# Kernel tuning notes

Measured on AMD Instinct MI355X. Metric: run time of the kernel, lower is better.

## Reference

```python
import jax, jax.numpy as jnp
import numpy as np
from jax import lax

T = 8  # hardcoded temporal length in the torch module

def _dwconv_t(z, w, b):
    # z: (N, C, T, 1); w: (C, 1, k, 1) depthwise; 'same' padding along T
    k = w.shape[2]
    p = (k - 1) // 2
    out = lax.conv_general_dilated(
        z, w, window_strides=(1, 1), padding=[(p, p), (0, 0)],
        feature_group_count=z.shape[1],
        dimension_numbers=('NCHW', 'OIHW', 'NCHW'))
    return out + b[None, :, None, None]


def setup_inputs() -> dict:
    key = jax.random.key(0)
    ks = jax.random.split(key, 13)
    C, IC, H, W, B = 1024, 512, 14, 14, 16
    s = lambda k, shp, scale: jax.random.normal(k, shp, dtype=jnp.float32) * scale
    return {
        'x':   s(ks[0], (B * T, C, H, W), 1.0),
        'w1':  s(ks[1], (IC, C, 1, 1), 0.03),
        'b1':  s(ks[2], (IC,), 0.02),
        'wb1': s(ks[3], (IC, 1, 1, 1), 0.3),
        'bb1': s(ks[4], (IC,), 0.02),
        'wb2': s(ks[5], (IC, 1, 3, 1), 0.3),
        'bb2': s(ks[6], (IC,), 0.02),
        'wb3': s(ks[7], (IC, 1, 5, 1), 0.3),
        'bb3': s(ks[8], (IC,), 0.02),
        'wb4': s(ks[9], (IC, 1, 7, 1), 0.3),
        'bb4': s(ks[10], (IC,), 0.02),
        'w2':  s(ks[11], (C, IC, 1, 1), 0.03),
        'b2':  s(ks[12], (C,), 0.02),
    }


def reference(x, w1, b1, wb1, bb1, wb2, bb2, wb3, bb3, wb4, bb4, w2, b2):
    BT, C, H, W = x.shape
    B = BT // T
    IC = w1.shape[0]
    # conv1: 1x1 pointwise conv == channel GEMM
    y = jnp.einsum('nchw,oc->nohw', x, w1[:, :, 0, 0]) + b1[None, :, None, None]
    # (B*T, IC, H, W) -> (B, T, IC, H, W) -> (B, H, W, IC, T) -> (B*H*W, IC, T, 1)
    z = y.reshape(B, T, IC, H, W).transpose(0, 3, 4, 2, 1).reshape(B * H * W, IC, T, 1)
    out = (_dwconv_t(z, wb1, bb1) + _dwconv_t(z, wb2, bb2)
           + _dwconv_t(z, wb3, bb3) + _dwconv_t(z, wb4, bb4))
    # (B*H*W, IC, T, 1) -> (B, H, W, IC, T) -> (B, T, IC, H, W) -> (B*T, IC, H, W)
    out = out.reshape(B, H, W, IC, T).transpose(0, 4, 3, 1, 2).reshape(BT, IC, H, W)
    # conv2: 1x1 pointwise conv back to C channels
    out = jnp.einsum('nihw,oi->nohw', out, w2[:, :, 0, 0]) + b2[None, :, None, None]
    return x + out
```

## Files before the change

kernel.cpp:

```cpp
#include <hip/hip_runtime.h>
#include <hip/hip_bf16.h>

typedef short short8 __attribute__((ext_vector_type(8)));
typedef float f32x4 __attribute__((ext_vector_type(4)));
typedef unsigned int uint;

#define CB   16
#define TT   8
#define CIN  1024
#define ICH  512
#define HWS  196
#define NPB  1568
#define NF   25088

static __device__ __forceinline__ unsigned short f2bf(float f) {
  __hip_bfloat16 h = __float2bfloat16(f); unsigned short u; __builtin_memcpy(&u, &h, 2); return u;
}

static __device__ __forceinline__ void stage16(const void* g, void* l) {
  __builtin_amdgcn_global_load_lds(
      (const __attribute__((address_space(1))) unsigned int*)(unsigned long long)g,
      (__attribute__((address_space(3))) unsigned int*)(unsigned int)(unsigned long long)l,
      16, 0, 0);
}

__global__ void k_prep(const float* __restrict__ x, __hip_bfloat16* __restrict__ xbT,
    const float* __restrict__ w1, const float* __restrict__ w2,
    const float* __restrict__ wb1, const float* __restrict__ bb1,
    const float* __restrict__ wb2, const float* __restrict__ bb2,
    const float* __restrict__ wb3, const float* __restrict__ bb3,
    const float* __restrict__ wb4, const float* __restrict__ bb4,
    __hip_bfloat16* __restrict__ w1b, __hip_bfloat16* __restrict__ w2b,
    float* __restrict__ weff, float* __restrict__ beff) {
  int bid = blockIdx.x;
  if (bid >= CB * TT * 16 * 4) {
    int idx = (bid - CB * TT * 16 * 4) * 256 + threadIdx.x;
    if (idx < CIN * ICH) {
      w1b[idx] = __float2bfloat16(w1[idx]);
      w2b[idx] = __float2bfloat16(w2[idx]);
    }
    if (idx < ICH) {
      float e[7];
#pragma unroll
      for (int u = 0; u < 7; u++) e[u] = wb4[idx * 7 + u];
#pragma unroll
      for (int u = 0; u < 5; u++) e[u + 1] += wb3[idx * 5 + u];
#pragma unroll
      for (int u = 0; u < 3; u++) e[u + 2] += wb2[idx * 3 + u];
      e[3] += wb1[idx];
#pragma unroll
      for (int u = 0; u < 7; u++) weff[idx * 8 + u] = e[u];
      weff[idx * 8 + 7] = 0.f;
      beff[idx] = bb1[idx] + bb2[idx] + bb3[idx] + bb4[idx];
    }
    return;
  }
  __shared__ float tile[64][51];
  int ht = bid & 3;
  int ct = (bid >> 2) & 15;
  int t  = (bid >> 6) & 7;
  int b  = bid >> 9;
  int c0 = ct * 64, h0 = ht * 49;
  const float* src = x + ((size_t)((b * TT + t) * CIN + c0)) * HWS + h0;
  for (int idx = threadIdx.x; idx < 64 * 49; idx += 256) {
    int r = idx / 49, q = idx - r * 49;
    tile[r][q] = src[(size_t)r * HWS + q];
  }
  __syncthreads();
  for (int idx = threadIdx.x; idx < 49 * 16; idx += 256) {
    int h = idx >> 4, g = idx & 15;
    ushort4 pk;
    pk.x = f2bf(tile[g * 4 + 0][h]);
    pk.y = f2bf(tile[g * 4 + 1][h]);
    pk.z = f2bf(tile[g * 4 + 2][h]);
    pk.w = f2bf(tile[g * 4 + 3][h]);
    size_t n1 = (size_t)(h0 + h) * TT + t;
    *(ushort4*)&xbT[((size_t)b * NPB + n1) * CIN + (c0 + g * 4)] = pk;
  }
}

template <int KD>
static __device__ __forceinline__ void gemm_core64(
    const __hip_bfloat16* __restrict__ Ar,
    const __hip_bfloat16* __restrict__ Br,
    __hip_bfloat16* As, __hip_bfloat16* Bs, f32x4 (&acc)[8][4]) {
  constexpr int NT = KD / 64;
  const int tid = threadIdx.x;
  const int lane = tid & 63, w = tid >> 6;
  const int wm = w >> 2, wn = w & 3;
  const int ln = lane & 15, lm = lane >> 4;
  const int srow = lane >> 3;
  const int schk = (lane & 7) ^ srow;
  const __hip_bfloat16* aS = Ar + (size_t)(w * 16 + srow) * KD + schk * 8;
  const __hip_bfloat16* bS = Br + (size_t)(w * 16 + srow) * KD + schk * 8;
  __hip_bfloat16* aD = As + (w * 16) * 64;
  __hip_bfloat16* bD = Bs + (w * 16) * 64;
  const int ck0 = ((lm) ^ (ln & 7)) * 8;
  const int ck1 = ((4 + lm) ^ (ln & 7)) * 8;
  int ra[8], rb[4];
#pragma unroll
  for (int mf = 0; mf < 8; mf++) ra[mf] = (mf * 32 + wm * 16 + ln) * 64;
#pragma unroll
  for (int nf = 0; nf < 4; nf++) rb[nf] = (wn * 64 + nf * 16 + ln) * 64;

#define STG_(src, dst, h, q, kt, buf) \
  stage16(src + (size_t)((h) * 128 + (q) * 8) * KD + (kt) * 64, \
          dst + (buf) * 16384 + ((h) * 128 + (q) * 8) * 64)

  STG_(bS, bD, 0, 0, 0, 0); STG_(bS, bD, 0, 1, 0, 0);
  STG_(bS, bD, 1, 0, 0, 0); STG_(bS, bD, 1, 1, 0, 0);
  STG_(aS, aD, 0, 0, 0, 0); STG_(aS, aD, 0, 1, 0, 0);
  STG_(aS, aD, 1, 0, 0, 0); STG_(aS, aD, 1, 1, 0, 0);

  short8 afA[4], afB[4], bfA[4], bfB[4];
  for (int t = 0; t < NT; t++) {
    const int buf = t & 1, nb = buf ^ 1;
    const bool has = (t + 1 < NT);
    const int bufo = buf * 16384;
    const __hip_bfloat16* Ab = As + bufo;
    const __hip_bfloat16* Bb = Bs + bufo;
    if (has) { STG_(bS, bD, 0, 0, t + 1, nb); STG_(bS, bD, 0, 1, t + 1, nb); }
    if (has) asm volatile("s_waitcnt vmcnt(4)" ::: "memory");
    else     asm volatile("s_waitcnt vmcnt(2)" ::: "memory");
    asm volatile("s_barrier" ::: "memory");
#pragma unroll
    for (int q = 0; q < 4; q++) afA[q] = *(const short8*)&Ab[ra[q] + ck0];
#pragma unroll
    for (int nf = 0; nf < 4; nf++) bfA[nf] = *(const short8*)&Bb[rb[nf] + ck0];
#pragma unroll
    for (int q = 0; q < 4; q++) afB[q] = *(const short8*)&Ab[ra[q] + ck1];
#pragma unroll
    for (int nf = 0; nf < 4; nf++) bfB[nf] = *(const short8*)&Bb[rb[nf] + ck1];
    asm volatile("s_waitcnt lgkmcnt(8)" ::: "memory");
    __builtin_amdgcn_sched_barrier(0);
    __builtin_amdgcn_s_setprio(1);
#pragma unroll
    for (int nf = 0; nf < 4; nf++)
#pragma unroll
      for (int q = 0; q < 4; q++)
        acc[q][nf] = __builtin_amdgcn_mfma_f32_16x16x32_bf16(afA[q], bfA[nf], acc[q][nf], 0, 0, 0);
    __builtin_amdgcn_s_setprio(0);
    if (has) { STG_(bS, bD, 1, 0, t + 1, nb); STG_(bS, bD, 1, 1, t + 1, nb); }
    asm volatile("s_waitcnt lgkmcnt(0)" ::: "memory");
    __builtin_amdgcn_sched_barrier(0);
    __builtin_amdgcn_s_setprio(1);
#pragma unroll
    for (int nf = 0; nf < 4; nf++)
#pragma unroll
      for (int q = 0; q < 4; q++)
        acc[q][nf] = __builtin_amdgcn_mfma_f32_16x16x32_bf16(afB[q], bfB[nf], acc[q][nf], 0, 0, 0);
    __builtin_amdgcn_s_setprio(0);
    if (has) { STG_(aS, aD, 0, 0, t + 1, nb); STG_(aS, aD, 0, 1, t + 1, nb); }
    if (has) asm volatile("s_waitcnt vmcnt(6)" ::: "memory");
    else     asm volatile("s_waitcnt vmcnt(0)" ::: "memory");
    asm volatile("s_barrier" ::: "memory");
#pragma unroll
    for (int q = 0; q < 4; q++) afA[q] = *(const short8*)&Ab[ra[4 + q] + ck0];
#pragma unroll
    for (int q = 0; q < 4; q++) afB[q] = *(const short8*)&Ab[ra[4 + q] + ck1];
    asm volatile("s_waitcnt lgkmcnt(4)" ::: "memory");
    __builtin_amdgcn_sched_barrier(0);
    __builtin_amdgcn_s_setprio(1);
#pragma unroll
    for (int nf = 0; nf < 4; nf++)
#pragma unroll
      for (int q = 0; q < 4; q++)
        acc[4 + q][nf] = __builtin_amdgcn_mfma_f32_16x16x32_bf16(afA[q], bfA[nf], acc[4 + q][nf], 0, 0, 0);
    __builtin_amdgcn_s_setprio(0);
    if (has) { STG_(aS, aD, 1, 0, t + 1, nb); STG_(aS, aD, 1, 1, t + 1, nb); }
    asm volatile("s_waitcnt lgkmcnt(0)" ::: "memory");
    __builtin_amdgcn_sched_barrier(0);
    asm volatile("s_barrier" ::: "memory");
    __builtin_amdgcn_s_setprio(1);
#pragma unroll
    for (int nf = 0; nf < 4; nf++)
#pragma unroll
      for (int q = 0; q < 4; q++)
        acc[4 + q][nf] = __builtin_amdgcn_mfma_f32_16x16x32_bf16(afB[q], bfB[nf], acc[4 + q][nf], 0, 0, 0);
    __builtin_amdgcn_s_setprio(0);
  }
#undef STG_
}

__global__ __launch_bounds__(512, 2) void k_gemm1(const __hip_bfloat16* __restrict__ xbT,
                                                  const __hip_bfloat16* __restrict__ w1b,
                                                  const float* __restrict__ b1,
                                                  const float* __restrict__ weff,
                                                  const float* __restrict__ beff,
                                                  __hip_bfloat16* __restrict__ dwT) {
  __shared__ __hip_bfloat16 As[2 * 256 * 64];
  __shared__ __hip_bfloat16 Bs[2 * 256 * 64];
  int xcd = blockIdx.x & 7, i = blockIdx.x >> 3;
  int id = (xcd < 4 ? xcd * 25 : 100 + (xcd - 4) * 24) + i;
  int rt = id >> 1, ot = id & 1;
  int n0 = rt * 256, o0 = ot * 256;
  f32x4 acc[8][4];
#pragma unroll
  for (int a = 0; a < 8; a++)
#pragma unroll
    for (int c = 0; c < 4; c++) acc[a][c] = (f32x4){0.f, 0.f, 0.f, 0.f};
  gemm_core64<1024>(xbT + (size_t)n0 * CIN, w1b + (size_t)o0 * CIN, As, Bs, acc);

  int tid = threadIdx.x, lane = tid & 63, w = tid >> 6;
  int wm = w >> 2, wn = w & 3, ln = lane & 15, lm = lane >> 4;
  bool hiT = (lm & 1);
#pragma unroll
  for (int nf = 0; nf < 4; nf++) {
    int o = o0 + wn * 64 + nf * 16 + ln;
    float e[7];
#pragma unroll
    for (int u = 0; u < 7; u++) e[u] = weff[o * 8 + u];
    float be = beff[o];
    float bo = b1[o];
#pragma unroll
    for (int mf = 0; mf < 8; mf++) {
      float av[4], pv[4];
#pragma unroll
      for (int j = 0; j < 4; j++) av[j] = acc[mf][nf][j] + bo;
#pragma unroll
      for (int j = 0; j < 4; j++) pv[j] = __shfl_xor(av[j], 16, 64);
      float ov[4];
      if (hiT) {
#pragma unroll
        for (int j = 0; j < 4; j++) {
          float s = be;
#pragma unroll
          for (int u = 0; u < 7; u++) {
            int ss = 4 + j + u - 3;
            if (ss >= 0 && ss < 8) s += e[u] * (ss < 4 ? pv[ss] : av[ss - 4]);
          }
          ov[j] = s;
        }
      } else {
#pragma unroll
        for (int j = 0; j < 4; j++) {
          float s = be;
#pragma unroll
          for (int u = 0; u < 7; u++) {
            int ss = j + u - 3;
            if (ss >= 0 && ss < 8) s += e[u] * (ss < 4 ? av[ss] : pv[ss - 4]);
          }
          ov[j] = s;
        }
      }
      int grow = n0 + mf * 32 + wm * 16 + ((lm >> 1) & 1) * 8;
      int gidx = grow >> 3;
      int gb = gidx / HWS, ghw = gidx - gb * HWS;
      int tb = hiT ? 4 : 0;
#pragma unroll
      for (int j = 0; j < 4; j++) {
        size_t rr = (size_t)gb * NPB + (size_t)(tb + j) * HWS + ghw;
        dwT[rr * ICH + o] = __float2bfloat16(ov[j]);
      }
    }
  }
}

__global__ __launch_bounds__(512, 2) void k_gemm2(const __hip_bfloat16* __restrict__ dwT,
                                                  const __hip_bfloat16* __restrict__ w2b,
                                                  const float* __restrict__ b2,
                                                  const float* __restrict__ xres,
                                                  float* __restrict__ out) {
  __shared__ __align__(16) char smem[131072];
  __hip_bfloat16* As = (__hip_bfloat16*)smem;
  __hip_bfloat16* Bs = (__hip_bfloat16*)(smem + 65536);
  int id = (blockIdx.x & 7) * 49 + (blockIdx.x >> 3);
  int nt = id >> 2, mt = id & 3;
  int n0 = nt * 256, m0 = mt * 256;
  f32x4 acc[8][4];
#pragma unroll
  for (int a = 0; a < 8; a++)
#pragma unroll
    for (int c = 0; c < 4; c++) acc[a][c] = (f32x4){0.f, 0.f, 0.f, 0.f};
  gemm_core64<512>(w2b + (size_t)m0 * ICH, dwT + (size_t)n0 * ICH, As, Bs, acc);

  int tid = threadIdx.x, lane = tid & 63, w = tid >> 6;
  int wm = w >> 2, wn = w & 3, ln = lane & 15, lm = lane >> 4;
  float* arr = (float*)smem;
  int fc = tid & 63, fr = tid >> 6;
  int n2 = n0 + fc * 4;
  int bb = n2 / NPB, r = n2 - bb * NPB;
  int t2 = r / HWS, hw = r - t2 * HWS;
  size_t base4 = ((size_t)((bb * TT + t2) * CIN)) * HWS + hw;
#pragma unroll
  for (int p = 0; p < 4; p++) {
    __syncthreads();
#pragma unroll
    for (int q2 = 0; q2 < 2; q2++) {
      int mf = p * 2 + q2;
#pragma unroll
      for (int nf = 0; nf < 4; nf++)
#pragma unroll
        for (int j = 0; j < 4; j++)
          arr[(q2 * 32 + wm * 16 + lm * 4 + j) * 260 + wn * 64 + nf * 16 + ln] = acc[mf][nf][j];
    }
    __syncthreads();
#pragma unroll
    for (int it = 0; it < 8; it++) {
      int o2l = it * 8 + fr;
      f32x4 v = *(const f32x4*)&arr[o2l * 260 + fc * 4];
      int o2 = m0 + p * 64 + o2l;
      float bo = b2[o2];
      size_t a = base4 + (size_t)o2 * HWS;
      float4 xr = *(const float4*)(xres + a);
      float4 ov = make_float4(v[0] + bo + xr.x, v[1] + bo + xr.y,
                              v[2] + bo + xr.z, v[3] + bo + xr.w);
      *(float4*)(out + a) = ov;
    }
  }
}

extern "C" void kernel_launch(void* const* d_in, const int* in_sizes, int n_in,
                              void* d_out, int out_size, void* d_ws, size_t ws_size,
                              hipStream_t stream) {
  const float* x   = (const float*)d_in[0];
  const float* w1  = (const float*)d_in[1];
  const float* b1  = (const float*)d_in[2];
  const float* wb1 = (const float*)d_in[3];
  const float* bb1 = (const float*)d_in[4];
  const float* wb2 = (const float*)d_in[5];
  const float* bb2 = (const float*)d_in[6];
  const float* wb3 = (const float*)d_in[7];
  const float* bb3 = (const float*)d_in[8];
  const float* wb4 = (const float*)d_in[9];
  const float* bb4 = (const float*)d_in[10];
  const float* w2  = (const float*)d_in[11];
  const float* b2  = (const float*)d_in[12];
  float* out = (float*)d_out;

  __hip_bfloat16* xbT = (__hip_bfloat16*)d_out;

  char* ws = (char*)d_ws;
  __hip_bfloat16* dwT = (__hip_bfloat16*)ws;
  __hip_bfloat16* w1b = (__hip_bfloat16*)(ws + 25690112);
  __hip_bfloat16* w2b = (__hip_bfloat16*)(ws + 25690112 + 1048576);
  float* weff = (float*)(ws + 25690112 + 2097152);
  float* beff = weff + 4096;

  k_prep<<<CB * TT * 16 * 4 + (CIN * ICH + 255) / 256, 256, 0, stream>>>(
      x, xbT, w1, w2, wb1, bb1, wb2, bb2, wb3, bb3, wb4, bb4, w1b, w2b, weff, beff);
  k_gemm1<<<196, 512, 0, stream>>>(xbT, w1b, b1, weff, beff, dwT);
  k_gemm2<<<392, 512, 0, stream>>>(dwT, w2b, b2, x, out);
}
```

Measured before the change: 125.8 us.

## Switch GEMM mainloop to BK=32 triple-buffered LDS pipeline with prefetch depth two

The shared GEMM core changes from a K-tile of 64 with double buffering to a K-tile of 32 with three LDS buffers, prefetching two tiles ahead. The XOR swizzle and the staging pattern are redone for 32-wide rows. Each iteration now needs one barrier instead of two, and LDS use per block drops from 128KB to 96KB. The aim is to hide global-load latency better and cut barrier stalls. The cost is twice as many loop iterations and less MFMA work per barrier interval.

```diff
diff --git a/kernel.cpp b/kernel.cpp
--- a/kernel.cpp
+++ b/kernel.cpp
@@ -80,67 +80,61 @@
 }
 
 template <int KD>
-static __device__ __forceinline__ void gemm_core64(
+static __device__ __forceinline__ void gemm_core32(
     const __hip_bfloat16* __restrict__ Ar,
     const __hip_bfloat16* __restrict__ Br,
     __hip_bfloat16* As, __hip_bfloat16* Bs, f32x4 (&acc)[8][4]) {
-  constexpr int NT = KD / 64;
+  constexpr int NT = KD / 32;
   const int tid = threadIdx.x;
   const int lane = tid & 63, w = tid >> 6;
   const int wm = w >> 2, wn = w & 3;
   const int ln = lane & 15, lm = lane >> 4;
-  const int srow = lane >> 3;
-  const int schk = (lane & 7) ^ srow;
+  const int srow = lane >> 2;
+  const int schk = (lane & 3) ^ ((lane >> 3) & 3);
   const __hip_bfloat16* aS = Ar + (size_t)(w * 16 + srow) * KD + schk * 8;
   const __hip_bfloat16* bS = Br + (size_t)(w * 16 + srow) * KD + schk * 8;
-  __hip_bfloat16* aD = As + (w * 16) * 64;
-  __hip_bfloat16* bD = Bs + (w * 16) * 64;
-  const int ck0 = ((lm) ^ (ln & 7)) * 8;
-  const int ck1 = ((4 + lm) ^ (ln & 7)) * 8;
+  __hip_bfloat16* aD = As + (w * 16) * 32;
+  __hip_bfloat16* bD = Bs + (w * 16) * 32;
+  const int slot = (lm ^ ((ln >> 1) & 3)) * 8;
   int ra[8], rb[4];
 #pragma unroll
-  for (int mf = 0; mf < 8; mf++) ra[mf] = (mf * 32 + wm * 16 + ln) * 64;
-#pragma unroll
-  for (int nf = 0; nf < 4; nf++) rb[nf] = (wn * 64 + nf * 16 + ln) * 64;
-
-#define STG_(src, dst, h, q, kt, buf) \
-  stage16(src + (size_t)((h) * 128 + (q) * 8) * KD + (kt) * 64, \
-          dst + (buf) * 16384 + ((h) * 128 + (q) * 8) * 64)
-
-  STG_(bS, bD, 0, 0, 0, 0); STG_(bS, bD, 0, 1, 0, 0);
-  STG_(bS, bD, 1, 0, 0, 0); STG_(bS, bD, 1, 1, 0, 0);
-  STG_(aS, aD, 0, 0, 0, 0); STG_(aS, aD, 0, 1, 0, 0);
-  STG_(aS, aD, 1, 0, 0, 0); STG_(aS, aD, 1, 1, 0, 0);
-
-  short8 afA[4], afB[4], bfA[4], bfB[4];
+  for (int mf = 0; mf < 8; mf++) ra[mf] = (mf * 32 + wm * 16 + ln) * 32 + slot;
+#pragma unroll
+  for (int nf = 0; nf < 4; nf++) rb[nf] = (wn * 64 + nf * 16 + ln) * 32 + slot;
+
+#define STG(src, dst, h, kt, buf) \
+  stage16(src + (size_t)((h) * 128) * KD + (kt) * 32, dst + (buf) * 8192 + ((h) * 128) * 32)
+
+  STG(bS, bD, 0, 0, 0); STG(bS, bD, 1, 0, 0); STG(aS, aD, 0, 0, 0); STG(aS, aD, 1, 0, 0);
+  STG(bS, bD, 0, 1, 1); STG(bS, bD, 1, 1, 1); STG(aS, aD, 0, 1, 1); STG(aS, aD, 1, 1, 1);
+  asm volatile("s_waitcnt vmcnt(4)" ::: "memory");
+  asm volatile("s_barrier" ::: "memory");
+
+  short8 afA[4], afB[4], bf[4];
   for (int t = 0; t < NT; t++) {
-    const int buf = t & 1, nb = buf ^ 1;
-    const bool has = (t + 1 < NT);
-    const int bufo = buf * 16384;
-    const __hip_bfloat16* Ab = As + bufo;
-    const __hip_bfloat16* Bb = Bs + bufo;
-    if (has) { STG_(bS, bD, 0, 0, t + 1, nb); STG_(bS, bD, 0, 1, t + 1, nb); }
-    if (has) asm volatile("s_waitcnt vmcnt(4)" ::: "memory");
-    else     asm volatile("s_waitcnt vmcnt(2)" ::: "memory");
-    asm volatile("s_barrier" ::: "memory");
-#pragma unroll
-    for (int q = 0; q < 4; q++) afA[q] = *(const short8*)&Ab[ra[q] + ck0];
-#pragma unroll
-    for (int nf = 0; nf < 4; nf++) bfA[nf] = *(const short8*)&Bb[rb[nf] + ck0];
-#pragma unroll
-    for (int q = 0; q < 4; q++) afB[q] = *(const short8*)&Ab[ra[q] + ck1];
-#pragma unroll
-    for (int nf = 0; nf < 4; nf++) bfB[nf] = *(const short8*)&Bb[rb[nf] + ck1];
-    asm volatile("s_waitcnt lgkmcnt(8)" ::: "memory");
+    const int bc = t % 3;
+    const bool has = (t + 2 < NT);
+    const int nb = (t + 2) % 3;
+    const __hip_bfloat16* Ab = As + bc * 8192;
+    const __hip_bfloat16* Bb = Bs + bc * 8192;
+    if (has) { STG(bS, bD, 0, t + 2, nb); STG(bS, bD, 1, t + 2, nb); }
+#pragma unroll
+    for (int q = 0; q < 4; q++) afA[q] = *(const short8*)&Ab[ra[q]];
+#pragma unroll
+    for (int nf = 0; nf < 4; nf++) bf[nf] = *(const short8*)&Bb[rb[nf]];
+    __builtin_amdgcn_sched_barrier(0);
+    if (has) { STG(aS, aD, 0, t + 2, nb); STG(aS, aD, 1, t + 2, nb); }
+#pragma unroll
+    for (int q = 0; q < 4; q++) afB[q] = *(const short8*)&Ab[ra[4 + q]];
+    asm volatile("s_waitcnt lgkmcnt(4)" ::: "memory");
     __builtin_amdgcn_sched_barrier(0);
     __builtin_amdgcn_s_setprio(1);
 #pragma unroll
     for (int nf = 0; nf < 4; nf++)
 #pragma unroll
       for (int q = 0; q < 4; q++)
-        acc[q][nf] = __builtin_amdgcn_mfma_f32_16x16x32_bf16(afA[q], bfA[nf], acc[q][nf], 0, 0, 0);
+        acc[q][nf] = __builtin_amdgcn_mfma_f32_16x16x32_bf16(afA[q], bf[nf], acc[q][nf], 0, 0, 0);
     __builtin_amdgcn_s_setprio(0);
-    if (has) { STG_(bS, bD, 1, 0, t + 1, nb); STG_(bS, bD, 1, 1, t + 1, nb); }
     asm volatile("s_waitcnt lgkmcnt(0)" ::: "memory");
     __builtin_amdgcn_sched_barrier(0);
     __builtin_amdgcn_s_setprio(1);
@@ -148,38 +142,15 @@
     for (int nf = 0; nf < 4; nf++)
 #pragma unroll
       for (int q = 0; q < 4; q++)
-        acc[q][nf] = __builtin_amdgcn_mfma_f32_16x16x32_bf16(afB[q], bfB[nf], acc[q][nf], 0, 0, 0);
+        acc[4 + q][nf] = __builtin_amdgcn_mfma_f32_16x16x32_bf16(afB[q], bf[nf], acc[4 + q][nf], 0, 0, 0);
     __builtin_amdgcn_s_setprio(0);
-    if (has) { STG_(aS, aD, 0, 0, t + 1, nb); STG_(aS, aD, 0, 1, t + 1, nb); }
-    if (has) asm volatile("s_waitcnt vmcnt(6)" ::: "memory");
-    else     asm volatile("s_waitcnt vmcnt(0)" ::: "memory");
-    asm volatile("s_barrier" ::: "memory");
-#pragma unroll
-    for (int q = 0; q < 4; q++) afA[q] = *(const short8*)&Ab[ra[4 + q] + ck0];
-#pragma unroll
-    for (int q = 0; q < 4; q++) afB[q] = *(const short8*)&Ab[ra[4 + q] + ck1];
-    asm volatile("s_waitcnt lgkmcnt(4)" ::: "memory");
-    __builtin_amdgcn_sched_barrier(0);
-    __builtin_amdgcn_s_setprio(1);
-#pragma unroll
-    for (int nf = 0; nf < 4; nf++)
-#pragma unroll
-      for (int q = 0; q < 4; q++)
-        acc[4 + q][nf] = __builtin_amdgcn_mfma_f32_16x16x32_bf16(afA[q], bfA[nf], acc[4 + q][nf], 0, 0, 0);
-    __builtin_amdgcn_s_setprio(0);
-    if (has) { STG_(aS, aD, 1, 0, t + 1, nb); STG_(aS, aD, 1, 1, t + 1, nb); }
-    asm volatile("s_waitcnt lgkmcnt(0)" ::: "memory");
-    __builtin_amdgcn_sched_barrier(0);
-    asm volatile("s_barrier" ::: "memory");
-    __builtin_amdgcn_s_setprio(1);
-#pragma unroll
-    for (int nf = 0; nf < 4; nf++)
-#pragma unroll
-      for (int q = 0; q < 4; q++)
-        acc[4 + q][nf] = __builtin_amdgcn_mfma_f32_16x16x32_bf16(afB[q], bfB[nf], acc[4 + q][nf], 0, 0, 0);
-    __builtin_amdgcn_s_setprio(0);
-  }
-#undef STG_
+    if (t + 1 < NT) {
+      if (has) asm volatile("s_waitcnt vmcnt(4)" ::: "memory");
+      else     asm volatile("s_waitcnt vmcnt(0)" ::: "memory");
+      asm volatile("s_barrier" ::: "memory");
+    }
+  }
+#undef STG
 }
 
 __global__ __launch_bounds__(512, 2) void k_gemm1(const __hip_bfloat16* __restrict__ xbT,
@@ -188,8 +159,8 @@
                                                   const float* __restrict__ weff,
                                                   const float* __restrict__ beff,
                                                   __hip_bfloat16* __restrict__ dwT) {
-  __shared__ __hip_bfloat16 As[2 * 256 * 64];
-  __shared__ __hip_bfloat16 Bs[2 * 256 * 64];
+  __shared__ __hip_bfloat16 As[3 * 256 * 32];
+  __shared__ __hip_bfloat16 Bs[3 * 256 * 32];
   int xcd = blockIdx.x & 7, i = blockIdx.x >> 3;
   int id = (xcd < 4 ? xcd * 25 : 100 + (xcd - 4) * 24) + i;
   int rt = id >> 1, ot = id & 1;
@@ -199,7 +170,7 @@
   for (int a = 0; a < 8; a++)
 #pragma unroll
     for (int c = 0; c < 4; c++) acc[a][c] = (f32x4){0.f, 0.f, 0.f, 0.f};
-  gemm_core64<1024>(xbT + (size_t)n0 * CIN, w1b + (size_t)o0 * CIN, As, Bs, acc);
+  gemm_core32<1024>(xbT + (size_t)n0 * CIN, w1b + (size_t)o0 * CIN, As, Bs, acc);
 
   int tid = threadIdx.x, lane = tid & 63, w = tid >> 6;
   int wm = w >> 2, wn = w & 3, ln = lane & 15, lm = lane >> 4;
@@ -261,9 +232,9 @@
                                                   const float* __restrict__ b2,
                                                   const float* __restrict__ xres,
                                                   float* __restrict__ out) {
-  __shared__ __align__(16) char smem[131072];
+  __shared__ __align__(16) char smem[98304];
   __hip_bfloat16* As = (__hip_bfloat16*)smem;
-  __hip_bfloat16* Bs = (__hip_bfloat16*)(smem + 65536);
+  __hip_bfloat16* Bs = (__hip_bfloat16*)(smem + 49152);
   int id = (blockIdx.x & 7) * 49 + (blockIdx.x >> 3);
   int nt = id >> 2, mt = id & 3;
   int n0 = nt * 256, m0 = mt * 256;
@@ -272,7 +243,7 @@
   for (int a = 0; a < 8; a++)
 #pragma unroll
     for (int c = 0; c < 4; c++) acc[a][c] = (f32x4){0.f, 0.f, 0.f, 0.f};
-  gemm_core64<512>(w2b + (size_t)m0 * ICH, dwT + (size_t)n0 * ICH, As, Bs, acc);
+  gemm_core32<512>(w2b + (size_t)m0 * ICH, dwT + (size_t)n0 * ICH, As, Bs, acc);
 
   int tid = threadIdx.x, lane = tid & 63, w = tid >> 6;
   int wm = w >> 2, wn = w & 3, ln = lane & 15, lm = lane >> 4;
```

After: 131.5 us. 1.05x slower.
